# Kernel optimization log

Measured on AMD Instinct MI355X. Metric: run time of the kernel, lower is better.

Reference implementation:

```python
import jax, jax.numpy as jnp
import numpy as np

N = 100000      # nodes
E = 1200000     # edges
D = 64          # feature dim
RW = 3          # round_window
L = 2           # num_layers
EPS = -1.0      # GIN init_eps -> (1+eps)*h + neighbor_sum == pure neighbor sum
LN_EPS = 1e-5   # torch LayerNorm default eps


def _ln(x):
    # LayerNorm over feature dim, elementwise_affine=False
    mu = jnp.mean(x, axis=-1, keepdims=True)
    var = jnp.var(x, axis=-1, keepdims=True)
    return (x - mu) * jax.lax.rsqrt(var + LN_EPS)


def _gin(h, src, dst):
    # DGL GINConv(None, 'sum'): (1+eps)*h_dst + sum_{src->dst} h_src
    agg = jax.ops.segment_sum(h[src], dst, num_segments=N)
    return (1.0 + EPS) * h + agg


def setup_inputs() -> dict:
    key = jax.random.key(0)
    k1, k2, k3, k4 = jax.random.split(key, 4)
    feature = jax.random.normal(k1, (N, D), dtype=jnp.float32)
    age = jax.random.randint(k2, (N,), 0, RW)
    src = jax.random.randint(k3, (E,), 0, N)
    dst = jax.random.randint(k4, (E,), 0, N)
    return {"feature": feature, "age": age, "src": src, "dst": dst}


def reference(feature, age, src, dst):
    hn = _ln(feature)  # normalize the (tiled) input features
    # window w keeps nodes with age >= w
    mask = (jnp.arange(RW)[:, None] <= age[None, :]).astype(hn.dtype)  # [RW, N]
    h0 = hn[None, :, :] * mask[:, :, None]  # [RW, N, D]
    windows = []
    for w in range(RW):  # small fixed round_window
        h = h0[w]
        feats = [h]
        for _ in range(L):
            h = jax.nn.relu(_ln(_gin(h, src, dst)))
            feats.append(h)
        windows.append(jnp.concatenate(feats, axis=1))  # [N, (L+1)*D]
    h_self = windows[0]
    # temporal_agg == 'mean_final'
    h_temp = jnp.mean(jnp.stack([windows[0] - windows[i] for i in range(1, RW)]), axis=0)
    return jnp.concatenate([h_self, h_temp], axis=1)  # [N, 2*(L+1)*D]
```

## Files before the change

kernel.cpp:

```cpp
#include <hip/hip_runtime.h>
#include <hip/hip_bf16.h>

constexpr int NN  = 100000;
constexpr int EE  = 1200000;
constexpr int D   = 64;
constexpr int CAP = 64;
constexpr int ZROW = NN;
constexpr float LN_EPS = 1e-5f;
constexpr int NXCD = 8;
constexpr int NPX  = (NN + NXCD - 1) / NXCD;
constexpr int FILL_GRP = 256;
constexpr int FILL_BLOCKS = NXCD * FILL_GRP;
constexpr int NAPW = (NN + 15) / 16;

__global__ void fillx_kernel(const int* __restrict__ src, const int* __restrict__ dst,
                             const unsigned* __restrict__ agePk, int* __restrict__ cnt,
                             int* __restrict__ packed) {
    int bid = blockIdx.x;
    int xcd = bid & 7;
    int grp = bid >> 3;
    int lo = xcd * NPX;
    int hi = min(lo + NPX, NN);
    int per = (EE + FILL_GRP - 1) / FILL_GRP;
    int e0 = grp * per;
    int e1 = min(e0 + per, EE);
    for (int e = e0 + (int)threadIdx.x; e < e1; e += (int)blockDim.x) {
        int d = dst[e];
        if (d >= lo && d < hi) {
            int slot = atomicAdd(&cnt[d], 1);
            if (slot < CAP) {
                int s = src[e];
                unsigned aw = agePk[s >> 4];
                int ag = (aw >> ((s & 15) * 2)) & 3;
                packed[(size_t)d * CAP + slot] = s | (ag << 17);
            }
        }
    }
}

__device__ __forceinline__ float2 bf22f2(ushort2 u) {
    float2 r;
    r.x = __uint_as_float((unsigned)u.x << 16);
    r.y = __uint_as_float((unsigned)u.y << 16);
    return r;
}

__device__ __forceinline__ ushort2 f2bf2(float2 v) {
    __hip_bfloat16 a = __float2bfloat16(v.x);
    __hip_bfloat16 b = __float2bfloat16(v.y);
    ushort2 u;
    u.x = *(const unsigned short*)&a;
    u.y = *(const unsigned short*)&b;
    return u;
}

__device__ __forceinline__ float2 ln_relu_pair(float2 a, bool relu) {
    float s = a.x + a.y;
    #pragma unroll
    for (int m = 1; m < 32; m <<= 1) s += __shfl_xor(s, m);
    float mu = s * (1.f / 64.f);
    float dx = a.x - mu, dy = a.y - mu;
    float q = dx * dx + dy * dy;
    #pragma unroll
    for (int m = 1; m < 32; m <<= 1) q += __shfl_xor(q, m);
    float rs = rsqrtf(q * (1.f / 64.f) + LN_EPS);
    float2 r;
    r.x = dx * rs;
    r.y = dy * rs;
    if (relu) { r.x = fmaxf(r.x, 0.f); r.y = fmaxf(r.y, 0.f); }
    return r;
}

__global__ void ln_kernel(const float* __restrict__ x, const int* __restrict__ age,
                          __hip_bfloat16* __restrict__ ybf,
                          __hip_bfloat16* __restrict__ A1bf, int* __restrict__ cnt,
                          unsigned* __restrict__ agePk, int nrows) {
    int gid  = blockIdx.x * blockDim.x + threadIdx.x;
    if (gid < NN) cnt[gid] = 0;
    if (gid < 192) {
        A1bf[(size_t)ZROW * 192 + gid] = __float2bfloat16(0.f);
        if (gid < 64) ybf[(size_t)ZROW * D + gid] = __float2bfloat16(0.f);
    }
    if (gid < NAPW) {
        unsigned w = 0;
        int base = gid * 16;
        #pragma unroll
        for (int k = 0; k < 16; ++k) {
            int idx = base + k;
            unsigned a = (idx < NN) ? (unsigned)age[idx] : 0u;
            w |= (a & 3u) << (2 * k);
        }
        agePk[gid] = w;
    }
    int row  = gid >> 6;
    int lane = gid & 63;
    if (row >= nrows) return;
    size_t i = (size_t)row * D + lane;
    float v = x[i];
    float s = v;
    #pragma unroll
    for (int m = 1; m < 64; m <<= 1) s += __shfl_xor(s, m);
    float mu = s * (1.f / 64.f);
    float d = v - mu;
    float q = d * d;
    #pragma unroll
    for (int m = 1; m < 64; m <<= 1) q += __shfl_xor(q, m);
    float r = d * rsqrtf(q * (1.f / 64.f) + LN_EPS);
    ybf[i] = __float2bfloat16(r);
}

__global__ void gather1_kernel(const __hip_bfloat16* __restrict__ hnbf,
                               const int* __restrict__ cnt,
                               const int* __restrict__ packed,
                               __hip_bfloat16* __restrict__ A1bf,
                               float* __restrict__ out) {
    int gid  = blockIdx.x * blockDim.x + threadIdx.x;
    int node = gid >> 6;
    int lane = gid & 63;
    if (node >= NN) return;
    int sl = lane & 31;
    int h  = lane >> 5;
    int n  = min(cnt[node], CAP);
    int nc4 = (n + 3) >> 2;
    int mc  = max(nc4 - 1, 0);
    const int* pl = packed + (size_t)node * CAP;
    float2 a0 = {0.f, 0.f}, a1 = {0.f, 0.f}, a2 = {0.f, 0.f};

    {
        int c0 = min(h, mc), c1 = min(h + 2, mc);
        int4 pa = *reinterpret_cast<const int4*>(pl + 4 * c0);
        int4 pb = *reinterpret_cast<const int4*>(pl + 4 * c1);
        int pA[4] = {pa.x, pa.y, pa.z, pa.w};
        int pB[4] = {pb.x, pb.y, pb.z, pb.w};
        #pragma unroll
        for (int k = 0; k < 8; ++k) {
            int i  = (k < 4) ? (4 * h + k) : (4 * (h + 2) + (k - 4));
            int pk = (k < 4) ? pA[k] : pB[k - 4];
            int idx = (i < n) ? (pk & 0x1FFFF) : ZROW;
            const ushort2* row = reinterpret_cast<const ushort2*>(
                hnbf + (size_t)idx * D);
            float2 v = bf22f2(row[sl]);
            int g = pk >> 17;
            a0.x += v.x; a0.y += v.y;
            if (g >= 1) { a1.x += v.x; a1.y += v.y; }
            if (g >= 2) { a2.x += v.x; a2.y += v.y; }
        }
    }
    for (int c = 4 + h; c < nc4; c += 2) {
        int4 pc = *reinterpret_cast<const int4*>(pl + 4 * c);
        int pC[4] = {pc.x, pc.y, pc.z, pc.w};
        #pragma unroll
        for (int k = 0; k < 4; ++k) {
            int i = 4 * c + k;
            int idx = (i < n) ? (pC[k] & 0x1FFFF) : ZROW;
            const ushort2* row = reinterpret_cast<const ushort2*>(
                hnbf + (size_t)idx * D);
            float2 v = bf22f2(row[sl]);
            int g = pC[k] >> 17;
            a0.x += v.x; a0.y += v.y;
            if (g >= 1) { a1.x += v.x; a1.y += v.y; }
            if (g >= 2) { a2.x += v.x; a2.y += v.y; }
        }
    }
    a0.x += __shfl_xor(a0.x, 32); a0.y += __shfl_xor(a0.y, 32);
    a1.x += __shfl_xor(a1.x, 32); a1.y += __shfl_xor(a1.y, 32);
    a2.x += __shfl_xor(a2.x, 32); a2.y += __shfl_xor(a2.y, 32);

    float2 r0 = ln_relu_pair(a0, true);
    float2 r1 = ln_relu_pair(a1, true);
    float2 r2 = ln_relu_pair(a2, true);

    ushort2* rw = reinterpret_cast<ushort2*>(A1bf + (size_t)node * (3 * D));
    float* ob = out + (size_t)node * 384;
    if (h == 0) {
        rw[sl] = f2bf2(r0);
        reinterpret_cast<float2*>(ob + 64)[sl] = r0;
    } else {
        rw[32 + sl] = f2bf2(r1);
        rw[64 + sl] = f2bf2(r2);
        float2 o4;
        o4.x = r0.x - 0.5f * (r1.x + r2.x);
        o4.y = r0.y - 0.5f * (r1.y + r2.y);
        reinterpret_cast<float2*>(ob + 256)[sl] = o4;
    }
}

__global__ void gather2_kernel(const __hip_bfloat16* __restrict__ hnbf,
                               const __hip_bfloat16* __restrict__ A1bf,
                               const int* __restrict__ cnt, const int* __restrict__ packed,
                               const int* __restrict__ age, float* __restrict__ out) {
    int gid  = blockIdx.x * blockDim.x + threadIdx.x;
    int node = gid >> 6;
    int lane = gid & 63;
    if (node >= NN) return;
    int sl = lane & 31;
    int h  = lane >> 5;
    int n  = min(cnt[node], CAP);
    int nc4 = (n + 3) >> 2;
    int mc  = max(nc4 - 1, 0);
    const int* pl = packed + (size_t)node * CAP;
    float2 a0 = {0.f, 0.f}, a1 = {0.f, 0.f}, a2 = {0.f, 0.f};

    {
        int c0 = min(h, mc), c1 = min(h + 2, mc);
        int4 pa = *reinterpret_cast<const int4*>(pl + 4 * c0);
        int4 pb = *reinterpret_cast<const int4*>(pl + 4 * c1);
        int pA[4] = {pa.x, pa.y, pa.z, pa.w};
        int pB[4] = {pb.x, pb.y, pb.z, pb.w};
        #pragma unroll
        for (int k = 0; k < 8; ++k) {
            int i  = (k < 4) ? (4 * h + k) : (4 * (h + 2) + (k - 4));
            int pk = (k < 4) ? pA[k] : pB[k - 4];
            int idx = (i < n) ? (pk & 0x1FFFF) : ZROW;
            const ushort2* row = reinterpret_cast<const ushort2*>(
                A1bf + (size_t)idx * (3 * D));
            float2 v0 = bf22f2(row[sl]);
            float2 v1 = bf22f2(row[32 + sl]);
            float2 v2 = bf22f2(row[64 + sl]);
            a0.x += v0.x; a0.y += v0.y;
            a1.x += v1.x; a1.y += v1.y;
            a2.x += v2.x; a2.y += v2.y;
        }
    }
    for (int c = 4 + h; c < nc4; c += 2) {
        int4 pc = *reinterpret_cast<const int4*>(pl + 4 * c);
        int pC[4] = {pc.x, pc.y, pc.z, pc.w};
        #pragma unroll
        for (int k = 0; k < 4; ++k) {
            int i = 4 * c + k;
            int idx = (i < n) ? (pC[k] & 0x1FFFF) : ZROW;
            const ushort2* row = reinterpret_cast<const ushort2*>(
                A1bf + (size_t)idx * (3 * D));
            float2 v0 = bf22f2(row[sl]);
            float2 v1 = bf22f2(row[32 + sl]);
            float2 v2 = bf22f2(row[64 + sl]);
            a0.x += v0.x; a0.y += v0.y;
            a1.x += v1.x; a1.y += v1.y;
            a2.x += v2.x; a2.y += v2.y;
        }
    }
    a0.x += __shfl_xor(a0.x, 32); a0.y += __shfl_xor(a0.y, 32);
    a1.x += __shfl_xor(a1.x, 32); a1.y += __shfl_xor(a1.y, 32);
    a2.x += __shfl_xor(a2.x, 32); a2.y += __shfl_xor(a2.y, 32);

    float2 h20 = ln_relu_pair(a0, true);
    float2 h21 = ln_relu_pair(a1, true);
    float2 h22 = ln_relu_pair(a2, true);

    float2 hnv = bf22f2(reinterpret_cast<const ushort2*>(
        hnbf + (size_t)node * D)[sl]);
    int ag = age[node];
    float f = 1.f - 0.5f * (float)((ag >= 1) + (ag >= 2));
    float* ob = out + (size_t)node * 384;
    if (h == 0) {
        reinterpret_cast<float2*>(ob)[sl] = hnv;
        reinterpret_cast<float2*>(ob + 128)[sl] = h20;
    } else {
        float2 o3, o5;
        o3.x = hnv.x * f;
        o3.y = hnv.y * f;
        o5.x = h20.x - 0.5f * (h21.x + h22.x);
        o5.y = h20.y - 0.5f * (h21.y + h22.y);
        reinterpret_cast<float2*>(ob + 192)[sl] = o3;
        reinterpret_cast<float2*>(ob + 320)[sl] = o5;
    }
}

extern "C" void kernel_launch(void* const* d_in, const int* in_sizes, int n_in,
                              void* d_out, int out_size, void* d_ws, size_t ws_size,
                              hipStream_t stream) {
    const float* feature = (const float*)d_in[0];
    const int*   age     = (const int*)d_in[1];
    const int*   src     = (const int*)d_in[2];
    const int*   dst     = (const int*)d_in[3];
    float* out = (float*)d_out;

    size_t nd1 = (size_t)(NN + 1) * D;
    __hip_bfloat16* hnbf = (__hip_bfloat16*)d_ws;
    __hip_bfloat16* A1bf = hnbf + nd1;
    int* cnt    = (int*)(A1bf + (size_t)(NN + 1) * 3 * D);
    int* packed = cnt + NN;
    unsigned* agePk = (unsigned*)(packed + (size_t)NN * CAP);

    ln_kernel<<<(int)(((size_t)NN * D + 255) / 256), 256, 0, stream>>>(
        feature, age, hnbf, A1bf, cnt, agePk, NN);
    fillx_kernel<<<FILL_BLOCKS, 256, 0, stream>>>(src, dst, agePk, cnt, packed);
    gather1_kernel<<<(NN * 64 + 255) / 256, 256, 0, stream>>>(hnbf, cnt, packed, A1bf, out);
    gather2_kernel<<<(NN * 64 + 255) / 256, 256, 0, stream>>>(hnbf, A1bf, cnt, packed,
                                                              age, out);
}
```

Baseline: 205.6 us.

## Interleave layer-1 windows per lane and co-schedule LayerNorm with edge bucketing

```diff
diff --git a/kernel.cpp b/kernel.cpp
--- a/kernel.cpp
+++ b/kernel.cpp
@@ -11,31 +11,78 @@
 constexpr int NPX  = (NN + NXCD - 1) / NXCD;
 constexpr int FILL_GRP = 256;
 constexpr int FILL_BLOCKS = NXCD * FILL_GRP;
+constexpr int LN_BLOCKS = (NN * D) / 256;
 constexpr int NAPW = (NN + 15) / 16;
 
-__global__ void fillx_kernel(const int* __restrict__ src, const int* __restrict__ dst,
-                             const unsigned* __restrict__ agePk, int* __restrict__ cnt,
-                             int* __restrict__ packed) {
+typedef unsigned uint3v __attribute__((ext_vector_type(3)));
+
+__global__ void prep_kernel(const int* __restrict__ age, int* __restrict__ cnt,
+                            unsigned* __restrict__ agePk,
+                            __hip_bfloat16* __restrict__ ybf,
+                            unsigned short* __restrict__ A1i) {
+    int gid = blockIdx.x * blockDim.x + threadIdx.x;
+    if (gid < NN) cnt[gid] = 0;
+    if (gid < NAPW) {
+        unsigned w = 0;
+        int base = gid * 16;
+        #pragma unroll
+        for (int k = 0; k < 16; ++k) {
+            int idx = base + k;
+            unsigned a = (idx < NN) ? (unsigned)age[idx] : 0u;
+            w |= (a & 3u) << (2 * k);
+        }
+        agePk[gid] = w;
+    }
+    if (gid < 192) {
+        A1i[(size_t)ZROW * 192 + gid] = 0;
+        if (gid < 64) ybf[(size_t)ZROW * D + gid] = __float2bfloat16(0.f);
+    }
+}
+
+__global__ void fill_ln_kernel(const int* __restrict__ src, const int* __restrict__ dst,
+                               const unsigned* __restrict__ agePk,
+                               const float* __restrict__ x,
+                               int* __restrict__ cnt, int* __restrict__ packed,
+                               __hip_bfloat16* __restrict__ ybf) {
     int bid = blockIdx.x;
-    int xcd = bid & 7;
-    int grp = bid >> 3;
-    int lo = xcd * NPX;
-    int hi = min(lo + NPX, NN);
-    int per = (EE + FILL_GRP - 1) / FILL_GRP;
-    int e0 = grp * per;
-    int e1 = min(e0 + per, EE);
-    for (int e = e0 + (int)threadIdx.x; e < e1; e += (int)blockDim.x) {
-        int d = dst[e];
-        if (d >= lo && d < hi) {
-            int slot = atomicAdd(&cnt[d], 1);
-            if (slot < CAP) {
-                int s = src[e];
-                unsigned aw = agePk[s >> 4];
-                int ag = (aw >> ((s & 15) * 2)) & 3;
-                packed[(size_t)d * CAP + slot] = s | (ag << 17);
+    if (bid < FILL_BLOCKS) {
+        int xcd = bid & 7;
+        int grp = bid >> 3;
+        int lo = xcd * NPX;
+        int hi = min(lo + NPX, NN);
+        int per = (EE + FILL_GRP - 1) / FILL_GRP;
+        int e0 = grp * per;
+        int e1 = min(e0 + per, EE);
+        for (int e = e0 + (int)threadIdx.x; e < e1; e += (int)blockDim.x) {
+            int d = dst[e];
+            if (d >= lo && d < hi) {
+                int slot = atomicAdd(&cnt[d], 1);
+                if (slot < CAP) {
+                    int s = src[e];
+                    unsigned aw = agePk[s >> 4];
+                    int ag = (aw >> ((s & 15) * 2)) & 3;
+                    packed[(size_t)d * CAP + slot] = s | (ag << 17);
+                }
             }
         }
-    }
+        return;
+    }
+    int gid  = (bid - FILL_BLOCKS) * (int)blockDim.x + (int)threadIdx.x;
+    int row  = gid >> 6;
+    int lane = gid & 63;
+    if (row >= NN) return;
+    size_t i = (size_t)row * D + lane;
+    float v = x[i];
+    float s = v;
+    #pragma unroll
+    for (int m = 1; m < 64; m <<= 1) s += __shfl_xor(s, m);
+    float mu = s * (1.f / 64.f);
+    float d = v - mu;
+    float q = d * d;
+    #pragma unroll
+    for (int m = 1; m < 64; m <<= 1) q += __shfl_xor(q, m);
+    float r = d * rsqrtf(q * (1.f / 64.f) + LN_EPS);
+    ybf[i] = __float2bfloat16(r);
 }
 
 __device__ __forceinline__ float2 bf22f2(ushort2 u) {
@@ -45,13 +92,13 @@
     return r;
 }
 
-__device__ __forceinline__ ushort2 f2bf2(float2 v) {
-    __hip_bfloat16 a = __float2bfloat16(v.x);
-    __hip_bfloat16 b = __float2bfloat16(v.y);
-    ushort2 u;
-    u.x = *(const unsigned short*)&a;
-    u.y = *(const unsigned short*)&b;
-    return u;
+__device__ __forceinline__ float bfu2f(unsigned u) {
+    return __uint_as_float(u << 16);
+}
+
+__device__ __forceinline__ unsigned short f2bfu(float v) {
+    __hip_bfloat16 b = __float2bfloat16(v);
+    return *(const unsigned short*)&b;
 }
 
 __device__ __forceinline__ float2 ln_relu_pair(float2 a, bool relu) {
@@ -71,48 +118,10 @@
     return r;
 }
 
-__global__ void ln_kernel(const float* __restrict__ x, const int* __restrict__ age,
-                          __hip_bfloat16* __restrict__ ybf,
-                          __hip_bfloat16* __restrict__ A1bf, int* __restrict__ cnt,
-                          unsigned* __restrict__ agePk, int nrows) {
-    int gid  = blockIdx.x * blockDim.x + threadIdx.x;
-    if (gid < NN) cnt[gid] = 0;
-    if (gid < 192) {
-        A1bf[(size_t)ZROW * 192 + gid] = __float2bfloat16(0.f);
-        if (gid < 64) ybf[(size_t)ZROW * D + gid] = __float2bfloat16(0.f);
-    }
-    if (gid < NAPW) {
-        unsigned w = 0;
-        int base = gid * 16;
-        #pragma unroll
-        for (int k = 0; k < 16; ++k) {
-            int idx = base + k;
-            unsigned a = (idx < NN) ? (unsigned)age[idx] : 0u;
-            w |= (a & 3u) << (2 * k);
-        }
-        agePk[gid] = w;
-    }
-    int row  = gid >> 6;
-    int lane = gid & 63;
-    if (row >= nrows) return;
-    size_t i = (size_t)row * D + lane;
-    float v = x[i];
-    float s = v;
-    #pragma unroll
-    for (int m = 1; m < 64; m <<= 1) s += __shfl_xor(s, m);
-    float mu = s * (1.f / 64.f);
-    float d = v - mu;
-    float q = d * d;
-    #pragma unroll
-    for (int m = 1; m < 64; m <<= 1) q += __shfl_xor(q, m);
-    float r = d * rsqrtf(q * (1.f / 64.f) + LN_EPS);
-    ybf[i] = __float2bfloat16(r);
-}
-
 __global__ void gather1_kernel(const __hip_bfloat16* __restrict__ hnbf,
                                const int* __restrict__ cnt,
                                const int* __restrict__ packed,
-                               __hip_bfloat16* __restrict__ A1bf,
+                               unsigned short* __restrict__ A1i,
                                float* __restrict__ out) {
     int gid  = blockIdx.x * blockDim.x + threadIdx.x;
     int node = gid >> 6;
@@ -170,14 +179,15 @@
     float2 r1 = ln_relu_pair(a1, true);
     float2 r2 = ln_relu_pair(a2, true);
 
-    ushort2* rw = reinterpret_cast<ushort2*>(A1bf + (size_t)node * (3 * D));
     float* ob = out + (size_t)node * 384;
     if (h == 0) {
-        rw[sl] = f2bf2(r0);
+        unsigned d0 = (unsigned)f2bfu(r0.x) | ((unsigned)f2bfu(r1.x) << 16);
+        unsigned d1 = (unsigned)f2bfu(r2.x) | ((unsigned)f2bfu(r0.y) << 16);
+        unsigned d2 = (unsigned)f2bfu(r1.y) | ((unsigned)f2bfu(r2.y) << 16);
+        uint3v w = {d0, d1, d2};
+        *reinterpret_cast<uint3v*>(A1i + (size_t)node * 192 + sl * 6) = w;
         reinterpret_cast<float2*>(ob + 64)[sl] = r0;
     } else {
-        rw[32 + sl] = f2bf2(r1);
-        rw[64 + sl] = f2bf2(r2);
         float2 o4;
         o4.x = r0.x - 0.5f * (r1.x + r2.x);
         o4.y = r0.y - 0.5f * (r1.y + r2.y);
@@ -186,7 +196,7 @@
 }
 
 __global__ void gather2_kernel(const __hip_bfloat16* __restrict__ hnbf,
-                               const __hip_bfloat16* __restrict__ A1bf,
+                               const unsigned short* __restrict__ A1i,
                                const int* __restrict__ cnt, const int* __restrict__ packed,
                                const int* __restrict__ age, float* __restrict__ out) {
     int gid  = blockIdx.x * blockDim.x + threadIdx.x;
@@ -212,14 +222,11 @@
             int i  = (k < 4) ? (4 * h + k) : (4 * (h + 2) + (k - 4));
             int pk = (k < 4) ? pA[k] : pB[k - 4];
             int idx = (i < n) ? (pk & 0x1FFFF) : ZROW;
-            const ushort2* row = reinterpret_cast<const ushort2*>(
-                A1bf + (size_t)idx * (3 * D));
-            float2 v0 = bf22f2(row[sl]);
-            float2 v1 = bf22f2(row[32 + sl]);
-            float2 v2 = bf22f2(row[64 + sl]);
-            a0.x += v0.x; a0.y += v0.y;
-            a1.x += v1.x; a1.y += v1.y;
-            a2.x += v2.x; a2.y += v2.y;
+            uint3v w = *reinterpret_cast<const uint3v*>(
+                A1i + (size_t)idx * 192 + sl * 6);
+            a0.x += bfu2f(w.x & 0xffffu);  a0.y += bfu2f(w.y >> 16);
+            a1.x += bfu2f(w.x >> 16);      a1.y += bfu2f(w.z & 0xffffu);
+            a2.x += bfu2f(w.y & 0xffffu);  a2.y += bfu2f(w.z >> 16);
         }
     }
     for (int c = 4 + h; c < nc4; c += 2) {
@@ -229,14 +236,11 @@
         for (int k = 0; k < 4; ++k) {
             int i = 4 * c + k;
             int idx = (i < n) ? (pC[k] & 0x1FFFF) : ZROW;
-            const ushort2* row = reinterpret_cast<const ushort2*>(
-                A1bf + (size_t)idx * (3 * D));
-            float2 v0 = bf22f2(row[sl]);
-            float2 v1 = bf22f2(row[32 + sl]);
-            float2 v2 = bf22f2(row[64 + sl]);
-            a0.x += v0.x; a0.y += v0.y;
-            a1.x += v1.x; a1.y += v1.y;
-            a2.x += v2.x; a2.y += v2.y;
+            uint3v w = *reinterpret_cast<const uint3v*>(
+                A1i + (size_t)idx * 192 + sl * 6);
+            a0.x += bfu2f(w.x & 0xffffu);  a0.y += bfu2f(w.y >> 16);
+            a1.x += bfu2f(w.x >> 16);      a1.y += bfu2f(w.z & 0xffffu);
+            a2.x += bfu2f(w.y & 0xffffu);  a2.y += bfu2f(w.z >> 16);
         }
     }
     a0.x += __shfl_xor(a0.x, 32); a0.y += __shfl_xor(a0.y, 32);
@@ -277,15 +281,15 @@
 
     size_t nd1 = (size_t)(NN + 1) * D;
     __hip_bfloat16* hnbf = (__hip_bfloat16*)d_ws;
-    __hip_bfloat16* A1bf = hnbf + nd1;
-    int* cnt    = (int*)(A1bf + (size_t)(NN + 1) * 3 * D);
+    unsigned short* A1i  = (unsigned short*)(hnbf + nd1);
+    int* cnt    = (int*)(A1i + (size_t)(NN + 1) * 192);
     int* packed = cnt + NN;
     unsigned* agePk = (unsigned*)(packed + (size_t)NN * CAP);
 
-    ln_kernel<<<(int)(((size_t)NN * D + 255) / 256), 256, 0, stream>>>(
-        feature, age, hnbf, A1bf, cnt, agePk, NN);
-    fillx_kernel<<<FILL_BLOCKS, 256, 0, stream>>>(src, dst, agePk, cnt, packed);
-    gather1_kernel<<<(NN * 64 + 255) / 256, 256, 0, stream>>>(hnbf, cnt, packed, A1bf, out);
-    gather2_kernel<<<(NN * 64 + 255) / 256, 256, 0, stream>>>(hnbf, A1bf, cnt, packed,
+    prep_kernel<<<(NN + 255) / 256, 256, 0, stream>>>(age, cnt, agePk, hnbf, A1i);
+    fill_ln_kernel<<<FILL_BLOCKS + LN_BLOCKS, 256, 0, stream>>>(
+        src, dst, agePk, feature, cnt, packed, hnbf);
+    gather1_kernel<<<(NN * 64 + 255) / 256, 256, 0, stream>>>(hnbf, cnt, packed, A1i, out);
+    gather2_kernel<<<(NN * 64 + 255) / 256, 256, 0, stream>>>(hnbf, A1i, cnt, packed,
                                                               age, out);
 }
```

New measurement: 203.3 us, median of 3. Within noise of the previous version (-1.1%).
